# Kernel tuning notes

Measured on AMD Instinct MI355X. Metric: run time of the kernel, lower is better.

The kernel has to match this reference:

```python
import jax, jax.numpy as jnp
import numpy as np

_CODEBOOK = np.array([
 [-1,-1,-1,-1,-1,-1,-1,-1,-1,-1],[-1,-1,-1,-1,1,1,-1,-1,-1,1],[-1,-1,-1,1,-1,-1,-1,-1,1,1],[-1,-1,-1,1,1,1,-1,-1,1,-1],
 [-1,-1,1,-1,-1,-1,-1,1,1,-1],[-1,-1,1,-1,1,1,-1,1,1,1],[-1,-1,1,1,-1,-1,-1,1,-1,1],[-1,-1,1,1,1,1,-1,1,-1,-1],
 [-1,1,-1,-1,-1,-1,1,1,-1,-1],[-1,1,-1,-1,1,1,1,1,-1,1],[-1,1,-1,1,-1,-1,1,1,1,1],[-1,1,-1,1,1,1,1,1,1,-1],
 [-1,1,1,-1,-1,-1,1,-1,1,-1],[-1,1,1,-1,1,1,1,-1,1,1],[-1,1,1,1,-1,-1,1,-1,-1,1],[-1,1,1,1,1,1,1,-1,-1,-1],
 [1,-1,-1,-1,-1,1,1,-1,-1,-1],[1,-1,-1,-1,1,-1,1,-1,-1,1],[1,-1,-1,1,-1,1,1,-1,1,1],[1,-1,-1,1,1,-1,1,-1,1,-1],
 [1,-1,1,-1,-1,1,1,1,1,-1],[1,-1,1,-1,1,-1,1,1,1,1],[1,-1,1,1,-1,1,1,1,-1,1],[1,-1,1,1,1,-1,1,1,-1,-1],
 [1,1,-1,-1,-1,1,-1,1,-1,-1],[1,1,-1,-1,1,-1,-1,1,-1,1],[1,1,-1,1,-1,1,-1,1,1,1],[1,1,-1,1,1,-1,-1,1,1,-1],
 [1,1,1,-1,-1,1,-1,-1,1,-1],[1,1,1,-1,1,-1,-1,-1,1,1],[1,1,1,1,-1,1,-1,-1,-1,1],[1,1,1,1,1,-1,-1,-1,-1,-1]],
 dtype=np.float32)

def setup_inputs() -> dict:
    key = jax.random.key(0)
    B, N, D = 64, 65536, 10
    signal = jax.random.normal(key, (B, N, D), dtype=jnp.float32)
    codebook = jnp.asarray(_CODEBOOK)  # [32, 10]
    return {"signal": signal, "codebook": codebook}

def reference(signal, codebook):
    # Euclidean distances to all 32 codewords via Gram trick: [B, N, 32]
    x2 = jnp.sum(signal * signal, axis=-1, keepdims=True)          # [B, N, 1]
    c2 = jnp.sum(codebook * codebook, axis=-1)                      # [32]
    xc = jnp.einsum('bnd,kd->bnk', signal, codebook)                # [B, N, 32]
    d2 = jnp.maximum(x2 + c2 - 2.0 * xc, 0.0)
    distances = jnp.sqrt(d2)
    soft_assignments = jax.nn.softmax(-distances, axis=2)           # [B, N, 32]
    most_like = jnp.argmax(soft_assignments, axis=2)                # [B, N]
    softdecision = codebook[most_like]                              # [B, N, 10]
    return softdecision
```

## Files before the change

### kernel.cpp

```cpp
#include <hip/hip_runtime.h>
#include <stdint.h>

#define PTS 256
#define DIM 10

static constexpr float CB[32][10] = {
 {-1,-1,-1,-1,-1,-1,-1,-1,-1,-1},{-1,-1,-1,-1,1,1,-1,-1,-1,1},{-1,-1,-1,1,-1,-1,-1,-1,1,1},{-1,-1,-1,1,1,1,-1,-1,1,-1},
 {-1,-1,1,-1,-1,-1,-1,1,1,-1},{-1,-1,1,-1,1,1,-1,1,1,1},{-1,-1,1,1,-1,-1,-1,1,-1,1},{-1,-1,1,1,1,1,-1,1,-1,-1},
 {-1,1,-1,-1,-1,-1,1,1,-1,-1},{-1,1,-1,-1,1,1,1,1,-1,1},{-1,1,-1,1,-1,-1,1,1,1,1},{-1,1,-1,1,1,1,1,1,1,-1},
 {-1,1,1,-1,-1,-1,1,-1,1,-1},{-1,1,1,-1,1,1,1,-1,1,1},{-1,1,1,1,-1,-1,1,-1,-1,1},{-1,1,1,1,1,1,1,-1,-1,-1},
 {1,-1,-1,-1,-1,1,1,-1,-1,-1},{1,-1,-1,-1,1,-1,1,-1,-1,1},{1,-1,-1,1,-1,1,1,-1,1,1},{1,-1,-1,1,1,-1,1,-1,1,-1},
 {1,-1,1,-1,-1,1,1,1,1,-1},{1,-1,1,-1,1,-1,1,1,1,1},{1,-1,1,1,-1,1,1,1,-1,1},{1,-1,1,1,1,-1,1,1,-1,-1},
 {1,1,-1,-1,-1,1,-1,1,-1,-1},{1,1,-1,-1,1,-1,-1,1,-1,1},{1,1,-1,1,-1,1,-1,1,1,1},{1,1,-1,1,1,-1,-1,1,1,-1},
 {1,1,1,-1,-1,1,-1,-1,1,-1},{1,1,1,-1,1,-1,-1,-1,1,1},{1,1,1,1,-1,1,-1,-1,-1,1},{1,1,1,1,1,-1,-1,-1,-1,-1}};

struct CBMasks { uint32_t m[32]; };
static constexpr CBMasks make_masks() {
    CBMasks r{};
    for (int k = 0; k < 32; ++k) {
        uint32_t mm = 0;
        for (int j = 0; j < DIM; ++j)
            if (CB[k][j] > 0.0f) mm |= (1u << j);
        r.m[k] = mm;
    }
    return r;
}
static constexpr CBMasks CBM = make_masks();

__global__ __launch_bounds__(PTS) void softdec_kernel(
    const float* __restrict__ sig, float* __restrict__ out)
{
    const size_t p = (size_t)blockIdx.x * PTS + threadIdx.x;

    const float2* __restrict__ gp = (const float2*)sig + p * 5;
    float x[DIM];
    #pragma unroll
    for (int q = 0; q < 5; ++q) {
        const float2 v = gp[q];
        x[2 * q]     = v.x;
        x[2 * q + 1] = v.y;
    }

    float    best = -1e30f;
    uint32_t bm   = 0u;
    #pragma unroll
    for (int k = 0; k < 32; ++k) {
        float s = 0.0f;
        #pragma unroll
        for (int j = 0; j < DIM; ++j)
            s = (CB[k][j] > 0.0f) ? (s + x[j]) : (s - x[j]);
        if (s > best) { best = s; bm = CBM.m[k]; }
    }

    float2* __restrict__ op = (float2*)out + p * 5;
    #pragma unroll
    for (int q = 0; q < 5; ++q) {
        float2 v;
        v.x = __uint_as_float(0xBF800000u ^ (((bm >> (2 * q))     & 1u) << 31));
        v.y = __uint_as_float(0xBF800000u ^ (((bm >> (2 * q + 1)) & 1u) << 31));
        op[q] = v;
    }
}

extern "C" void kernel_launch(void* const* d_in, const int* in_sizes, int n_in,
                              void* d_out, int out_size, void* d_ws, size_t ws_size,
                              hipStream_t stream) {
    const float* sig = (const float*)d_in[0];
    float* out = (float*)d_out;
    const int total  = in_sizes[0];
    const int pts    = total / DIM;
    const int blocks = pts / PTS;
    softdec_kernel<<<blocks, PTS, 0, stream>>>(sig, out);
}
```

Baseline: 281.8 us.

## Stage input and output through shared memory for coalesced float4 global access

Each block now loads its contiguous slab of 256 points into LDS with coalesced float4 loads, computes the best codeword per point from LDS, stores the chosen mask in LDS, and then writes the output slab with coalesced float4 stores. The old per-thread 40-byte-strided float2 accesses left each wavefront's loads and stores spread across many cache lines. The change adds two barriers, LDS traffic with possible bank conflicts on the stride-10 reads, and integer divide work when building the output.

```diff
diff --git a/kernel.cpp b/kernel.cpp
--- a/kernel.cpp
+++ b/kernel.cpp
@@ -1,8 +1,10 @@
 #include <hip/hip_runtime.h>
 #include <stdint.h>
 
-#define PTS 256
-#define DIM 10
+#define PTS    256
+#define DIM    10
+#define FLOATS (PTS * DIM)
+#define VECS   (FLOATS / 4)
 
 static constexpr float CB[32][10] = {
  {-1,-1,-1,-1,-1,-1,-1,-1,-1,-1},{-1,-1,-1,-1,1,1,-1,-1,-1,1},{-1,-1,-1,1,-1,-1,-1,-1,1,1},{-1,-1,-1,1,1,1,-1,-1,1,-1},
@@ -30,16 +32,24 @@
 __global__ __launch_bounds__(PTS) void softdec_kernel(
     const float* __restrict__ sig, float* __restrict__ out)
 {
-    const size_t p = (size_t)blockIdx.x * PTS + threadIdx.x;
+    __shared__ float    sIn[FLOATS];
+    __shared__ uint32_t sMask[PTS];
 
-    const float2* __restrict__ gp = (const float2*)sig + p * 5;
+    const int    tid  = threadIdx.x;
+    const size_t base = (size_t)blockIdx.x * FLOATS;
+
+    const float4* __restrict__ gin  = (const float4*)(sig + base);
+    float4*                    sIn4 = (float4*)sIn;
+    #pragma unroll
+    for (int it = 0; it < 3; ++it) {
+        const int i = tid + it * PTS;
+        if (i < VECS) sIn4[i] = gin[i];
+    }
+    __syncthreads();
+
     float x[DIM];
     #pragma unroll
-    for (int q = 0; q < 5; ++q) {
-        const float2 v = gp[q];
-        x[2 * q]     = v.x;
-        x[2 * q + 1] = v.y;
-    }
+    for (int j = 0; j < DIM; ++j) x[j] = sIn[tid * DIM + j];
 
     float    best = -1e30f;
     uint32_t bm   = 0u;
@@ -52,13 +62,26 @@
         if (s > best) { best = s; bm = CBM.m[k]; }
     }
 
-    float2* __restrict__ op = (float2*)out + p * 5;
+    sMask[tid] = bm;
+    __syncthreads();
+
+    float4* __restrict__ gout = (float4*)(out + base);
     #pragma unroll
-    for (int q = 0; q < 5; ++q) {
-        float2 v;
-        v.x = __uint_as_float(0xBF800000u ^ (((bm >> (2 * q))     & 1u) << 31));
-        v.y = __uint_as_float(0xBF800000u ^ (((bm >> (2 * q + 1)) & 1u) << 31));
-        op[q] = v;
+    for (int it = 0; it < 3; ++it) {
+        const int i = tid + it * PTS;
+        if (i < VECS) {
+            float4 v;
+            float* vv = (float*)&v;
+            #pragma unroll
+            for (int j = 0; j < 4; ++j) {
+                const int gg = 4 * i + j;
+                const int pp = gg / DIM;
+                const int cc = gg - pp * DIM;
+                vv[j] = __uint_as_float(
+                    0xBF800000u ^ (((sMask[pp] >> cc) & 1u) << 31));
+            }
+            gout[i] = v;
+        }
     }
 }
 
```

New measurement: 284.2 us. About the same (+0.9%).

## Persistent blocks with LDS-staged coalesced float4 loads, register prefetch, nontemporal stores

Applied to the files above, without the earlier changes.

Switches to a fixed grid of 2048 persistent blocks, each looping over several 256-point chunks. Inputs are loaded as coalesced float4 vectors and prefetched into registers for the next chunk, then staged through double-buffered LDS. The resulting codeword masks are written back as coalesced float4 nontemporal stores. The goal is to replace the stride-10 float2 accesses with fully coalesced wide transactions and to overlap loads with compute, at the cost of two barriers per chunk and more LDS use.

```diff
diff --git a/kernel.cpp b/kernel.cpp
--- a/kernel.cpp
+++ b/kernel.cpp
@@ -1,8 +1,13 @@
 #include <hip/hip_runtime.h>
 #include <stdint.h>
 
-#define PTS 256
-#define DIM 10
+#define PTS     256
+#define DIM     10
+#define FLOATS  (PTS * DIM)
+#define VECS    (FLOATS / 4)
+#define GRID    2048
+
+typedef float f32x4 __attribute__((ext_vector_type(4)));
 
 static constexpr float CB[32][10] = {
  {-1,-1,-1,-1,-1,-1,-1,-1,-1,-1},{-1,-1,-1,-1,1,1,-1,-1,-1,1},{-1,-1,-1,1,-1,-1,-1,-1,1,1},{-1,-1,-1,1,1,1,-1,-1,1,-1},
@@ -27,38 +32,84 @@
 }
 static constexpr CBMasks CBM = make_masks();
 
+__device__ __forceinline__ void barrier_lds_only() {
+    asm volatile("s_waitcnt lgkmcnt(0)" ::: "memory");
+    __builtin_amdgcn_s_barrier();
+    asm volatile("" ::: "memory");
+}
+
 __global__ __launch_bounds__(PTS) void softdec_kernel(
-    const float* __restrict__ sig, float* __restrict__ out)
+    const float* __restrict__ sig, float* __restrict__ out, int nc)
 {
-    const size_t p = (size_t)blockIdx.x * PTS + threadIdx.x;
+    __shared__ float    sIn [2][FLOATS];
+    __shared__ uint32_t sMask[2][PTS];
 
-    const float2* __restrict__ gp = (const float2*)sig + p * 5;
-    float x[DIM];
-    #pragma unroll
-    for (int q = 0; q < 5; ++q) {
-        const float2 v = gp[q];
-        x[2 * q]     = v.x;
-        x[2 * q + 1] = v.y;
+    const int tid = threadIdx.x;
+    const int c0  = blockIdx.x * nc;
+
+    float4 nxt0, nxt1, nxt2;
+    {
+        const float4* __restrict__ g = (const float4*)(sig + (size_t)c0 * FLOATS);
+        nxt0 = g[tid];
+        nxt1 = g[tid + PTS];
+        nxt2 = g[(tid + 2 * PTS) < VECS ? (tid + 2 * PTS) : (VECS - 1)];
     }
 
-    float    best = -1e30f;
-    uint32_t bm   = 0u;
-    #pragma unroll
-    for (int k = 0; k < 32; ++k) {
-        float s = 0.0f;
+    for (int t = 0; t < nc; ++t) {
+        const int buf = t & 1;
+
+        float4* s4 = (float4*)sIn[buf];
+        s4[tid]       = nxt0;
+        s4[tid + PTS] = nxt1;
+        if (tid < VECS - 2 * PTS) s4[tid + 2 * PTS] = nxt2;
+
+        if (t + 1 < nc) {
+            const float4* __restrict__ g =
+                (const float4*)(sig + (size_t)(c0 + t + 1) * FLOATS);
+            nxt0 = g[tid];
+            nxt1 = g[tid + PTS];
+            nxt2 = g[(tid + 2 * PTS) < VECS ? (tid + 2 * PTS) : (VECS - 1)];
+        }
+
+        barrier_lds_only();
+
+        float x[DIM];
         #pragma unroll
-        for (int j = 0; j < DIM; ++j)
-            s = (CB[k][j] > 0.0f) ? (s + x[j]) : (s - x[j]);
-        if (s > best) { best = s; bm = CBM.m[k]; }
-    }
+        for (int j = 0; j < DIM; ++j) x[j] = sIn[buf][tid * DIM + j];
 
-    float2* __restrict__ op = (float2*)out + p * 5;
-    #pragma unroll
-    for (int q = 0; q < 5; ++q) {
-        float2 v;
-        v.x = __uint_as_float(0xBF800000u ^ (((bm >> (2 * q))     & 1u) << 31));
-        v.y = __uint_as_float(0xBF800000u ^ (((bm >> (2 * q + 1)) & 1u) << 31));
-        op[q] = v;
+        float    best = -1e30f;
+        uint32_t bm   = 0u;
+        #pragma unroll
+        for (int k = 0; k < 32; ++k) {
+            float s = 0.0f;
+            #pragma unroll
+            for (int j = 0; j < DIM; ++j)
+                s = (CB[k][j] > 0.0f) ? (s + x[j]) : (s - x[j]);
+            if (s > best) { best = s; bm = CBM.m[k]; }
+        }
+        sMask[buf][tid] = bm;
+
+        barrier_lds_only();
+
+        f32x4* __restrict__ gout = (f32x4*)(out + (size_t)(c0 + t) * FLOATS);
+        #pragma unroll
+        for (int it = 0; it < 3; ++it) {
+            const int i = tid + it * PTS;
+            if (it < 2 || i < VECS) {
+                const int gg = 4 * i;
+                const int p0 = gg / DIM;
+                const int cc = gg - p0 * DIM;
+                const uint32_t m0 = sMask[buf][p0];
+                const uint32_t m1 = sMask[buf][(p0 + 1 < PTS) ? (p0 + 1) : p0];
+                const uint32_t mm = (m0 >> cc) | (m1 << (DIM - cc));
+                f32x4 v;
+                v.x = __uint_as_float(0xBF800000u ^ ((mm        & 1u) << 31));
+                v.y = __uint_as_float(0xBF800000u ^ (((mm >> 1) & 1u) << 31));
+                v.z = __uint_as_float(0xBF800000u ^ (((mm >> 2) & 1u) << 31));
+                v.w = __uint_as_float(0xBF800000u ^ (((mm >> 3) & 1u) << 31));
+                __builtin_nontemporal_store(v, gout + i);
+            }
+        }
     }
 }
 
@@ -69,6 +120,9 @@
     float* out = (float*)d_out;
     const int total  = in_sizes[0];
     const int pts    = total / DIM;
-    const int blocks = pts / PTS;
-    softdec_kernel<<<blocks, PTS, 0, stream>>>(sig, out);
+    const int chunks = pts / PTS;
+    int grid, nc;
+    if (chunks % GRID == 0) { grid = GRID;   nc = chunks / GRID; }
+    else                    { grid = chunks; nc = 1; }
+    softdec_kernel<<<grid, PTS, 0, stream>>>(sig, out, nc);
 }
```

Result: slower. 294.5 us (+4.5%).

## Stage coalesced float4 loads via LDS with persistent waves and register prefetch

Applied to the files above, without the earlier changes.

Replaces the one-point-per-thread kernel, which made strided float2 accesses, with a persistent grid of wave-sized work units. Each wave loads 128 points with fully coalesced float4 loads into shared memory and prefetches the next unit into registers. Each lane then computes two points. Output is written as coalesced float4 stores, with the packed masks redistributed across lanes via ds_bpermute. This targets memory-access efficiency on a bandwidth-bound kernel, in exchange for LDS traffic, bank conflicts on the 20-float stride reads, and more register use.

```diff
diff --git a/kernel.cpp b/kernel.cpp
--- a/kernel.cpp
+++ b/kernel.cpp
@@ -1,8 +1,13 @@
 #include <hip/hip_runtime.h>
 #include <stdint.h>
 
-#define PTS 256
-#define DIM 10
+#define DIM        10
+#define WPTS       128
+#define WFLOATS    (WPTS * DIM)
+#define WVECS      (WFLOATS / 4)
+#define WAVES      4
+#define THREADS    (WAVES * 64)
+#define GRID       2048
 
 static constexpr float CB[32][10] = {
  {-1,-1,-1,-1,-1,-1,-1,-1,-1,-1},{-1,-1,-1,-1,1,1,-1,-1,-1,1},{-1,-1,-1,1,-1,-1,-1,-1,1,1},{-1,-1,-1,1,1,1,-1,-1,1,-1},
@@ -27,20 +32,7 @@
 }
 static constexpr CBMasks CBM = make_masks();
 
-__global__ __launch_bounds__(PTS) void softdec_kernel(
-    const float* __restrict__ sig, float* __restrict__ out)
-{
-    const size_t p = (size_t)blockIdx.x * PTS + threadIdx.x;
-
-    const float2* __restrict__ gp = (const float2*)sig + p * 5;
-    float x[DIM];
-    #pragma unroll
-    for (int q = 0; q < 5; ++q) {
-        const float2 v = gp[q];
-        x[2 * q]     = v.x;
-        x[2 * q + 1] = v.y;
-    }
-
+__device__ __forceinline__ uint32_t argmax_mask(const float* __restrict__ x) {
     float    best = -1e30f;
     uint32_t bm   = 0u;
     #pragma unroll
@@ -51,14 +43,77 @@
             s = (CB[k][j] > 0.0f) ? (s + x[j]) : (s - x[j]);
         if (s > best) { best = s; bm = CBM.m[k]; }
     }
+    return bm;
+}
 
-    float2* __restrict__ op = (float2*)out + p * 5;
-    #pragma unroll
-    for (int q = 0; q < 5; ++q) {
-        float2 v;
-        v.x = __uint_as_float(0xBF800000u ^ (((bm >> (2 * q))     & 1u) << 31));
-        v.y = __uint_as_float(0xBF800000u ^ (((bm >> (2 * q + 1)) & 1u) << 31));
-        op[q] = v;
+__global__ __launch_bounds__(THREADS) void softdec_kernel(
+    const float* __restrict__ sig, float* __restrict__ out, int totw)
+{
+    __shared__ float sIn[WAVES][WFLOATS];
+
+    const int lane = threadIdx.x & 63;
+    const int wv   = threadIdx.x >> 6;
+    const int nw   = GRID * WAVES;
+    float* __restrict__ sW = sIn[wv];
+
+    const float4* __restrict__ gin = (const float4*)sig;
+
+    int w = blockIdx.x * WAVES + wv;
+
+    float4 p0, p1, p2, p3, p4;
+    {
+        const float4* __restrict__ g = gin + (size_t)w * WVECS;
+        p0 = g[lane];       p1 = g[lane + 64];  p2 = g[lane + 128];
+        p3 = g[lane + 192]; p4 = g[lane + 256];
+    }
+
+    while (w < totw) {
+        float4* __restrict__ s4 = (float4*)sW;
+        s4[lane]       = p0;  s4[lane +  64] = p1;  s4[lane + 128] = p2;
+        s4[lane + 192] = p3;  s4[lane + 256] = p4;
+
+        const int wn = w + nw;
+        if (wn < totw) {
+            const float4* __restrict__ g = gin + (size_t)wn * WVECS;
+            p0 = g[lane];       p1 = g[lane + 64];  p2 = g[lane + 128];
+            p3 = g[lane + 192]; p4 = g[lane + 256];
+        }
+
+        const float4* __restrict__ sp = (const float4*)(sW + lane * 2 * DIM);
+        const float4 a0 = sp[0], a1 = sp[1], a2 = sp[2], a3 = sp[3], a4 = sp[4];
+        float xA[DIM], xB[DIM];
+        xA[0]=a0.x; xA[1]=a0.y; xA[2]=a0.z; xA[3]=a0.w;
+        xA[4]=a1.x; xA[5]=a1.y; xA[6]=a1.z; xA[7]=a1.w;
+        xA[8]=a2.x; xA[9]=a2.y;
+        xB[0]=a2.z; xB[1]=a2.w;
+        xB[2]=a3.x; xB[3]=a3.y; xB[4]=a3.z; xB[5]=a3.w;
+        xB[6]=a4.x; xB[7]=a4.y; xB[8]=a4.z; xB[9]=a4.w;
+
+        const uint32_t pk = argmax_mask(xA) | (argmax_mask(xB) << DIM);
+
+        float4* __restrict__ gout = (float4*)out + (size_t)w * WVECS;
+        #pragma unroll
+        for (int q = 0; q < 5; ++q) {
+            const int v  = q * 64 + lane;
+            const int gg = 4 * v;
+            const int pA = gg / DIM;
+            const int cc = gg - pA * DIM;
+            const int pB = (pA + 1 < WPTS) ? (pA + 1) : (WPTS - 1);
+            const uint32_t pkA = (uint32_t)__builtin_amdgcn_ds_bpermute(
+                                     (pA >> 1) << 2, (int)pk);
+            const uint32_t pkB = (uint32_t)__builtin_amdgcn_ds_bpermute(
+                                     (pB >> 1) << 2, (int)pk);
+            const uint32_t A = (pkA >> ((pA & 1) * DIM)) & 0x3FFu;
+            const uint32_t B = (pkB >> ((pB & 1) * DIM)) & 0x3FFu;
+            const uint32_t mm = (A >> cc) | (B << (DIM - cc));
+            float4 o;
+            o.x = __uint_as_float(0xBF800000u ^ ((mm        & 1u) << 31));
+            o.y = __uint_as_float(0xBF800000u ^ (((mm >> 1) & 1u) << 31));
+            o.z = __uint_as_float(0xBF800000u ^ (((mm >> 2) & 1u) << 31));
+            o.w = __uint_as_float(0xBF800000u ^ (((mm >> 3) & 1u) << 31));
+            gout[v] = o;
+        }
+        w = wn;
     }
 }
 
@@ -67,8 +122,8 @@
                               hipStream_t stream) {
     const float* sig = (const float*)d_in[0];
     float* out = (float*)d_out;
-    const int total  = in_sizes[0];
-    const int pts    = total / DIM;
-    const int blocks = pts / PTS;
-    softdec_kernel<<<blocks, PTS, 0, stream>>>(sig, out);
+    const int total = in_sizes[0];
+    const int pts   = total / DIM;
+    const int totw  = pts / WPTS;
+    softdec_kernel<<<GRID, THREADS, 0, stream>>>(sig, out, totw);
 }
```

Result: no change. 284.1 us (+0.8%).
